# Kernel tuning notes

Measured on AMD Instinct MI355X. Metric: run time of the kernel, lower is better.

The kernel has to match this reference:

```python
import jax, jax.numpy as jnp
import numpy as np

BIGNET_DIM = 1024
N_LAYERS = 18   # 6 blocks * 3 QLoRALinear
N_LN = 5
GROUPS = 64     # 1024 / group_size(16)
GS = 16
RANK = 32
BATCH = 16384
EPS = 1e-5


def dequant(qw, scale):
    # qw: [O, G, gs] int 0..15, scale: [O, G] per-group max-abs norm
    w = (qw.astype(jnp.float32) / 15.0 * 2.0 - 1.0) * scale[..., None]
    return w.reshape(qw.shape[0], -1)  # [O, I]


def qlora_linear(x, qw, scale, b, a_w, b_w):
    w = dequant(qw, scale)                      # [O, I]
    base = x @ w.T + b                          # [N, O]
    lora = (x @ a_w.T) @ b_w.T                  # [N, r] @ [r, O]
    return base + lora


def layernorm(h, g, b):
    mu = h.mean(-1, keepdims=True)
    var = jnp.mean((h - mu) ** 2, -1, keepdims=True)
    return (h - mu) * jax.lax.rsqrt(var + EPS) * g + b


def setup_inputs() -> dict:
    key = jax.random.key(0)
    ks = jax.random.split(key, 8)
    x = jax.random.normal(ks[0], (BATCH, BIGNET_DIM), jnp.float32)
    qw = jax.random.randint(ks[1], (N_LAYERS, BIGNET_DIM, GROUPS, GS), 0, 16, jnp.int32)
    scale = jax.random.uniform(ks[2], (N_LAYERS, BIGNET_DIM, GROUPS), jnp.float32) * 0.05
    bias = jax.random.normal(ks[3], (N_LAYERS, BIGNET_DIM), jnp.float32) * 0.02
    la = jax.random.normal(ks[4], (N_LAYERS, RANK, BIGNET_DIM), jnp.float32) * (2.0 / BIGNET_DIM) ** 0.5
    # note: torch zero-inits lora_b; use small random values so the LoRA path is testable
    lb = jax.random.normal(ks[5], (N_LAYERS, BIGNET_DIM, RANK), jnp.float32) * 0.01
    ln_w = jnp.ones((N_LN, BIGNET_DIM), jnp.float32)
    ln_b = jnp.zeros((N_LN, BIGNET_DIM), jnp.float32)
    return {"x": x, "scale": scale, "bias": bias, "la": la, "lb": lb,
            "ln_w": ln_w, "ln_b": ln_b, "qw": qw}


def reference(x, scale, bias, la, lb, ln_w, ln_b, qw):
    h = x
    li = 0
    for blk in range(6):
        r = h
        for j in range(3):
            h = qlora_linear(h, qw[li], scale[li], bias[li], la[li], lb[li])
            li += 1
            if j < 2:
                h = jax.nn.relu(h)
        h = h + r
        if blk < 5:
            h = layernorm(h, ln_w[blk], ln_b[blk])
    return h
```

## Files before the change

kernel.cpp:

```cpp
#include <hip/hip_runtime.h>

typedef unsigned short UST;
typedef __attribute__((ext_vector_type(8))) __bf16 bf16x8;
typedef __attribute__((ext_vector_type(4))) float f32x4;

__device__ __forceinline__ float bf2f(UST u) {
    union { unsigned int i; float f; } v; v.i = ((unsigned int)u) << 16; return v.f;
}
__device__ __forceinline__ UST f2bf(float f) {
    union { float f; unsigned int i; } v; v.f = f;
    return (UST)((v.i + 0x7fffu + ((v.i >> 16) & 1u)) >> 16);
}

__device__ __forceinline__ void gl2lds16(const UST* g, UST* l) {
    __builtin_amdgcn_global_load_lds(
        (const __attribute__((address_space(1))) unsigned int*)g,
        (__attribute__((address_space(3))) unsigned int*)l, 16, 0, 0);
}

#define WB4 asm volatile("s_waitcnt vmcnt(4)\n\ts_barrier" ::: "memory")
#define WB0 asm volatile("s_waitcnt vmcnt(0)\n\ts_barrier" ::: "memory")
#define LGB asm volatile("s_waitcnt lgkmcnt(0)\n\ts_barrier" ::: "memory")

__global__ __launch_bounds__(256) void prep_w(
    const int* __restrict__ qw, const float* __restrict__ scale,
    const float* __restrict__ la, const float* __restrict__ lb,
    UST* __restrict__ wp)
{
    int l = blockIdx.x, ot = blockIdx.y, it = blockIdx.z;
    __shared__ float buf[8192];
    __shared__ float sc_s[128 * 8];
    int t = threadIdx.x;
    int wave = t >> 6, lane = t & 63;
    int wm = wave >> 1, wn = wave & 1;
    int la15 = lane & 15, qa = lane >> 4;

    {
        int e = t * 4;
        int o = e >> 3, g = e & 7;
        const float* sb = scale + ((size_t)l * 1024 + ot * 128 + o) * 64 + it * 8 + g;
        *(float4*)&sc_s[e] = *(const float4*)sb;
    }

    float* last = buf;
    {
        const float* laB = la + (size_t)l * 32 * 1024 + it * 128;
        #pragma unroll
        for (int p = 0; p < 4; p++) {
            int e = t * 4 + p * 1024;
            int r = e >> 7, i0 = e & 127;
            float4 v = *(const float4*)(laB + (size_t)r * 1024 + i0);
            last[(i0 + 0) * 33 + r] = v.x;
            last[(i0 + 1) * 33 + r] = v.y;
            last[(i0 + 2) * 33 + r] = v.z;
            last[(i0 + 3) * 33 + r] = v.w;
        }
    }

    bf16x8 af[4];
    const float* lbL = lb + ((size_t)l * 1024 + ot * 128 + wm * 64 + la15) * 32 + qa * 8;
    #pragma unroll
    for (int mi = 0; mi < 4; mi++) {
        float4 u0 = *(const float4*)(lbL + mi * 16 * 32);
        float4 u1 = *(const float4*)(lbL + mi * 16 * 32 + 4);
        union { bf16x8 v; UST u[8]; } A;
        A.u[0] = f2bf(u0.x); A.u[1] = f2bf(u0.y); A.u[2] = f2bf(u0.z); A.u[3] = f2bf(u0.w);
        A.u[4] = f2bf(u1.x); A.u[5] = f2bf(u1.y); A.u[6] = f2bf(u1.z); A.u[7] = f2bf(u1.w);
        af[mi] = A.v;
    }

    __syncthreads();

    bf16x8 bfr[4];
    #pragma unroll
    for (int ni = 0; ni < 4; ni++) {
        int iloc = wn * 64 + ni * 16 + la15;
        const float* pp = &last[iloc * 33 + qa * 8];
        union { bf16x8 v; UST u[8]; } B;
        #pragma unroll
        for (int j = 0; j < 8; j++) B.u[j] = f2bf(pp[j]);
        bfr[ni] = B.v;
    }

    f32x4 acc[4][4];
    #pragma unroll
    for (int mi = 0; mi < 4; mi++)
        #pragma unroll
        for (int ni = 0; ni < 4; ni++) {
            acc[mi][ni] = (f32x4){0.f, 0.f, 0.f, 0.f};
            acc[mi][ni] = __builtin_amdgcn_mfma_f32_16x16x32_bf16(
                af[mi], bfr[ni], acc[mi][ni], 0, 0, 0);
        }

    __syncthreads();

    float* cs = buf;
    int cc = t & 15, rw = t >> 4;
    UST* wL = wp + (size_t)l * 1048576;
    const int* qL = qw + (size_t)l * 1048576;
    #pragma unroll
    for (int h = 0; h < 2; ++h) {
        int4 qd[4][2];
        #pragma unroll
        for (int g = 0; g < 4; g++) {
            int rl = g * 16 + rw;
            const int* qrow = qL + (size_t)(ot * 128 + h * 64 + rl) * 1024
                              + it * 128 + cc * 8;
            qd[g][0] = *(const int4*)qrow;
            qd[g][1] = *(const int4*)(qrow + 4);
        }
        if (wm == h) {
            #pragma unroll
            for (int mi = 0; mi < 4; mi++)
                #pragma unroll
                for (int ni = 0; ni < 4; ni++) {
                    int colx = (wn * 64 + ni * 16 + la15) ^ (qa << 4);
                    #pragma unroll
                    for (int r2 = 0; r2 < 4; r2++) {
                        int rl = mi * 16 + qa * 4 + r2;
                        cs[rl * 128 + colx] = acc[mi][ni][r2];
                    }
                }
        }
        LGB;
        #pragma unroll
        for (int g = 0; g < 4; ++g) {
            int rl = g * 16 + rw;
            int swz = ((rl >> 2) & 3) << 2;
            int gr0 = ((cc * 2) ^ swz) * 4;
            float4 v0 = *(const float4*)&cs[rl * 128 + gr0];
            float4 v1 = *(const float4*)&cs[rl * 128 + gr0 + 4];
            float s = sc_s[(h * 64 + rl) * 8 + (cc >> 1)];
            float t2 = s * (2.0f / 15.0f);
            float o0 = fmaf((float)qd[g][0].x, t2, v0.x - s);
            float o1 = fmaf((float)qd[g][0].y, t2, v0.y - s);
            float o2 = fmaf((float)qd[g][0].z, t2, v0.z - s);
            float o3 = fmaf((float)qd[g][0].w, t2, v0.w - s);
            float o4 = fmaf((float)qd[g][1].x, t2, v1.x - s);
            float o5 = fmaf((float)qd[g][1].y, t2, v1.y - s);
            float o6 = fmaf((float)qd[g][1].z, t2, v1.z - s);
            float o7 = fmaf((float)qd[g][1].w, t2, v1.w - s);
            uint4 pk;
            pk.x = (unsigned)f2bf(o0) | ((unsigned)f2bf(o1) << 16);
            pk.y = (unsigned)f2bf(o2) | ((unsigned)f2bf(o3) << 16);
            pk.z = (unsigned)f2bf(o4) | ((unsigned)f2bf(o5) << 16);
            pk.w = (unsigned)f2bf(o6) | ((unsigned)f2bf(o7) << 16);
            *(uint4*)&wL[(size_t)(ot * 128 + h * 64 + rl) * 1024 + it * 128 + cc * 8] = pk;
        }
        LGB;
    }
}

__global__ __launch_bounds__(256) void f32_to_bf16(const float* __restrict__ x,
                                                   UST* __restrict__ o)
{
    size_t i = ((size_t)blockIdx.x * 256 + threadIdx.x) * 4;
    float4 v = *(const float4*)(x + i);
    *(ushort4*)(o + i) = make_ushort4(f2bf(v.x), f2bf(v.y), f2bf(v.z), f2bf(v.w));
}

#define BK 32

__global__ __launch_bounds__(512, 2) void gemm_ep(
    const UST* __restrict__ X, const UST* __restrict__ W,
    const float* __restrict__ bias,
    UST* __restrict__ outb, const UST* __restrict__ resid,
    float* __restrict__ outf, int mode)
{
    const int K = 1024;
    __shared__ UST smem[32768];
    int tid = threadIdx.x;
    int wave = tid >> 6, lane = tid & 63;
    int wm = wave >> 1, wn = wave & 1;
    int la15 = lane & 15, qa = lane >> 4;

    int bid = blockIdx.x;
    int xcd = bid & 7, idx = bid >> 3;
    int bm = xcd * 8 + (idx & 7);
    int bn = idx >> 3;

    int c0 = tid, c1 = tid + 512;
    int r0 = c0 >> 2, k0c = ((c0 & 3) ^ ((r0 >> 1) & 3)) * 8;
    int r1 = c1 >> 2, k1c = ((c1 & 3) ^ ((r1 >> 1) & 3)) * 8;
    const UST* gA0 = X + (size_t)(bm * 256 + r0) * K + k0c;
    const UST* gA1 = X + (size_t)(bm * 256 + r1) * K + k1c;
    const UST* gB0 = W + (size_t)(bn * 256 + r0) * K + k0c;
    const UST* gB1 = W + (size_t)(bn * 256 + r1) * K + k1c;

    int offA[4], offB[8];
    #pragma unroll
    for (int i = 0; i < 4; i++) {
        int ra = wm * 64 + i * 16 + la15;
        offA[i] = ra * 32 + ((qa ^ ((ra >> 1) & 3)) * 8);
    }
    #pragma unroll
    for (int i = 0; i < 8; i++) {
        int rb = wn * 128 + i * 16 + la15;
        offB[i] = rb * 32 + ((qa ^ ((rb >> 1) & 3)) * 8);
    }

    f32x4 acc[4][8];
    #pragma unroll
    for (int i = 0; i < 4; i++)
        #pragma unroll
        for (int j = 0; j < 8; j++) acc[i][j] = (f32x4){0.f, 0.f, 0.f, 0.f};

    auto issue = [&](int kk, int buf) {
        UST* dA = smem + buf * 16384;
        UST* dB = dA + 8192;
        gl2lds16(gA0 + kk, dA + c0 * 8);
        gl2lds16(gA1 + kk, dA + c1 * 8);
        gl2lds16(gB0 + kk, dB + c0 * 8);
        gl2lds16(gB1 + kk, dB + c1 * 8);
    };
    auto compute = [&](int buf) {
        const UST* pA = smem + buf * 16384;
        const UST* pB = pA + 8192;
        bf16x8 af[4], bfr[8];
        #pragma unroll
        for (int mi = 0; mi < 4; mi++) af[mi] = *(const bf16x8*)&pA[offA[mi]];
        #pragma unroll
        for (int ni = 0; ni < 8; ni++) bfr[ni] = *(const bf16x8*)&pB[offB[ni]];
        #pragma unroll
        for (int mi = 0; mi < 4; mi++)
            #pragma unroll
            for (int ni = 0; ni < 8; ni++)
                acc[mi][ni] = __builtin_amdgcn_mfma_f32_16x16x32_bf16(
                    af[mi], bfr[ni], acc[mi][ni], 0, 0, 0);
    };

    issue(0, 0);
    #pragma unroll 2
    for (int it = 0; it < 31; ++it) {
        int cur = it & 1;
        issue((it + 1) * BK, cur ^ 1);
        WB4;
        compute(cur);
        LGB;
    }
    WB0;
    compute(1);
    LGB;

    float* cs = (float*)smem;
    int cc = tid & 31, rw = tid >> 5;
    int gcolb = bn * 256 + cc * 8;
    float4 bv0 = *(const float4*)&bias[gcolb];
    float4 bv1 = *(const float4*)&bias[gcolb + 4];

    #pragma unroll
    for (int h = 0; h < 4; ++h) {
        if (wm == h) {
            #pragma unroll
            for (int mi = 0; mi < 4; mi++)
                #pragma unroll
                for (int ni = 0; ni < 8; ni++) {
                    int colx = (wn * 128 + ni * 16 + la15) ^ (qa << 4);
                    #pragma unroll
                    for (int r2 = 0; r2 < 4; r2++) {
                        int rl = mi * 16 + qa * 4 + r2;
                        cs[rl * 256 + colx] = acc[mi][ni][r2];
                    }
                }
        }
        LGB;
        #pragma unroll
        for (int g = 0; g < 4; ++g) {
            int rl = g * 16 + rw;
            int swz = ((rl >> 2) & 3) << 2;
            int gr0 = ((cc * 2) ^ swz) * 4;
            float4 v0 = *(const float4*)&cs[rl * 256 + gr0];
            float4 v1 = *(const float4*)&cs[rl * 256 + gr0 + 4];
            float o0 = v0.x + bv0.x, o1 = v0.y + bv0.y;
            float o2 = v0.z + bv0.z, o3 = v0.w + bv0.w;
            float o4 = v1.x + bv1.x, o5 = v1.y + bv1.y;
            float o6 = v1.z + bv1.z, o7 = v1.w + bv1.w;
            if (mode == 0) {
                o0 = fmaxf(o0, 0.f); o1 = fmaxf(o1, 0.f);
                o2 = fmaxf(o2, 0.f); o3 = fmaxf(o3, 0.f);
                o4 = fmaxf(o4, 0.f); o5 = fmaxf(o5, 0.f);
                o6 = fmaxf(o6, 0.f); o7 = fmaxf(o7, 0.f);
            }
            int grow = bm * 256 + h * 64 + rl;
            size_t base = (size_t)grow * 1024 + gcolb;
            if (mode != 0) {
                ushort4 rv0 = *(const ushort4*)&resid[base];
                ushort4 rv1 = *(const ushort4*)&resid[base + 4];
                o0 += bf2f(rv0.x); o1 += bf2f(rv0.y);
                o2 += bf2f(rv0.z); o3 += bf2f(rv0.w);
                o4 += bf2f(rv1.x); o5 += bf2f(rv1.y);
                o6 += bf2f(rv1.z); o7 += bf2f(rv1.w);
            }
            if (mode == 2) {
                *(float4*)&outf[base] = make_float4(o0, o1, o2, o3);
                *(float4*)&outf[base + 4] = make_float4(o4, o5, o6, o7);
            } else {
                uint4 pk;
                pk.x = (unsigned)f2bf(o0) | ((unsigned)f2bf(o1) << 16);
                pk.y = (unsigned)f2bf(o2) | ((unsigned)f2bf(o3) << 16);
                pk.z = (unsigned)f2bf(o4) | ((unsigned)f2bf(o5) << 16);
                pk.w = (unsigned)f2bf(o6) | ((unsigned)f2bf(o7) << 16);
                *(uint4*)&outb[base] = pk;
            }
        }
        LGB;
    }
}

__global__ __launch_bounds__(256) void ln_only(
    const UST* __restrict__ s, UST* __restrict__ r,
    const float* __restrict__ g, const float* __restrict__ b)
{
    int wave = threadIdx.x >> 6, lane = threadIdx.x & 63;
    int row = blockIdx.x * 4 + wave;
    const UST* sp = s + (size_t)row * 1024;
    UST* rp = r + (size_t)row * 1024;

    float v[16];
    float sum = 0.f, ss = 0.f;
    #pragma unroll
    for (int k = 0; k < 4; k++) {
        ushort4 hv = *(const ushort4*)(sp + k * 256 + lane * 4);
        float a0 = bf2f(hv.x), a1 = bf2f(hv.y), a2 = bf2f(hv.z), a3 = bf2f(hv.w);
        v[k * 4 + 0] = a0; v[k * 4 + 1] = a1; v[k * 4 + 2] = a2; v[k * 4 + 3] = a3;
        sum += a0 + a1 + a2 + a3;
        ss += a0 * a0 + a1 * a1 + a2 * a2 + a3 * a3;
    }
    #pragma unroll
    for (int off = 32; off > 0; off >>= 1) {
        sum += __shfl_down(sum, off, 64);
        ss  += __shfl_down(ss, off, 64);
    }
    sum = __shfl(sum, 0, 64);
    ss  = __shfl(ss, 0, 64);
    float mean = sum * (1.0f / 1024.0f);
    float var = ss * (1.0f / 1024.0f) - mean * mean;
    float rstd = rsqrtf(var + 1e-5f);

    #pragma unroll
    for (int k = 0; k < 4; k++) {
        int c = k * 256 + lane * 4;
        float4 gv = *(const float4*)(g + c);
        float4 bv = *(const float4*)(b + c);
        ushort4 o;
        o.x = f2bf((v[k * 4 + 0] - mean) * rstd * gv.x + bv.x);
        o.y = f2bf((v[k * 4 + 1] - mean) * rstd * gv.y + bv.y);
        o.z = f2bf((v[k * 4 + 2] - mean) * rstd * gv.z + bv.z);
        o.w = f2bf((v[k * 4 + 3] - mean) * rstd * gv.w + bv.w);
        *(ushort4*)(rp + c) = o;
    }
}

extern "C" void kernel_launch(void* const* d_in, const int* in_sizes, int n_in,
                              void* d_out, int out_size, void* d_ws, size_t ws_size,
                              hipStream_t stream) {
    const float* x     = (const float*)d_in[0];
    const float* scale = (const float*)d_in[1];
    const float* bias  = (const float*)d_in[2];
    const float* la    = (const float*)d_in[3];
    const float* lb    = (const float*)d_in[4];
    const float* ln_w  = (const float*)d_in[5];
    const float* ln_b  = (const float*)d_in[6];
    const int*   qw    = (const int*)d_in[7];

    const int M = in_sizes[0] / 1024;
    const size_t WPB = (size_t)18 * 1024 * 1024 * 2;
    const size_t ACT = (size_t)M * 1024 * 2;

    UST* wp = (UST*)d_ws;
    UST* A  = (UST*)((char*)d_ws + WPB);
    UST* Cb = (UST*)((char*)d_ws + WPB + ACT);
    UST* Bb = (UST*)d_out;

    prep_w<<<dim3(18, 8, 8), 256, 0, stream>>>(qw, scale, la, lb, wp);
    f32_to_bf16<<<(M * 1024) / (256 * 4), 256, 0, stream>>>(x, A);

    int nblk = (M / 256) * 4;
    int li = 0;
    for (int blk = 0; blk < 6; ++blk) {
        gemm_ep<<<nblk, 512, 0, stream>>>(
            A, wp + (size_t)li * 1024 * 1024, bias + li * 1024, Bb, nullptr, nullptr, 0);
        li++;
        gemm_ep<<<nblk, 512, 0, stream>>>(
            Bb, wp + (size_t)li * 1024 * 1024, bias + li * 1024, Cb, nullptr, nullptr, 0);
        li++;
        if (blk < 5) {
            gemm_ep<<<nblk, 512, 0, stream>>>(
                Cb, wp + (size_t)li * 1024 * 1024, bias + li * 1024, Bb, A, nullptr, 1);
            li++;
            ln_only<<<M / 4, 256, 0, stream>>>(Bb, A, ln_w + blk * 1024, ln_b + blk * 1024);
        } else {
            gemm_ep<<<nblk, 512, 0, stream>>>(
                Cb, wp + (size_t)li * 1024 * 1024, bias + li * 1024, nullptr, A,
                (float*)d_out, 2);
            li++;
        }
    }
}
```

Baseline: 940.9 us.

## Shrink GEMM tile to 128x256 with 256-thread blocks and raise MFMA priority

```diff
diff --git a/kernel.cpp b/kernel.cpp
--- a/kernel.cpp
+++ b/kernel.cpp
@@ -18,7 +18,7 @@
         (__attribute__((address_space(3))) unsigned int*)l, 16, 0, 0);
 }
 
-#define WB4 asm volatile("s_waitcnt vmcnt(4)\n\ts_barrier" ::: "memory")
+#define WB6 asm volatile("s_waitcnt vmcnt(6)\n\ts_barrier" ::: "memory")
 #define WB0 asm volatile("s_waitcnt vmcnt(0)\n\ts_barrier" ::: "memory")
 #define LGB asm volatile("s_waitcnt lgkmcnt(0)\n\ts_barrier" ::: "memory")
 
@@ -161,14 +161,14 @@
 
 #define BK 32
 
-__global__ __launch_bounds__(512, 2) void gemm_ep(
+__global__ __launch_bounds__(256, 2) void gemm_ep(
     const UST* __restrict__ X, const UST* __restrict__ W,
     const float* __restrict__ bias,
     UST* __restrict__ outb, const UST* __restrict__ resid,
     float* __restrict__ outf, int mode)
 {
     const int K = 1024;
-    __shared__ UST smem[32768];
+    __shared__ UST smem[24576];
     int tid = threadIdx.x;
     int wave = tid >> 6, lane = tid & 63;
     int wm = wave >> 1, wn = wave & 1;
@@ -176,16 +176,23 @@
 
     int bid = blockIdx.x;
     int xcd = bid & 7, idx = bid >> 3;
-    int bm = xcd * 8 + (idx & 7);
-    int bn = idx >> 3;
-
-    int c0 = tid, c1 = tid + 512;
-    int r0 = c0 >> 2, k0c = ((c0 & 3) ^ ((r0 >> 1) & 3)) * 8;
-    int r1 = c1 >> 2, k1c = ((c1 & 3) ^ ((r1 >> 1) & 3)) * 8;
-    const UST* gA0 = X + (size_t)(bm * 256 + r0) * K + k0c;
-    const UST* gA1 = X + (size_t)(bm * 256 + r1) * K + k1c;
-    const UST* gB0 = W + (size_t)(bn * 256 + r0) * K + k0c;
-    const UST* gB1 = W + (size_t)(bn * 256 + r1) * K + k1c;
+    int bm = xcd * 16 + (idx & 15);
+    int bn = idx >> 4;
+
+    int a0 = tid, a1 = tid + 256;
+    int rA0 = a0 >> 2, kA0 = ((a0 & 3) ^ ((rA0 >> 1) & 3)) * 8;
+    int rA1 = a1 >> 2, kA1 = ((a1 & 3) ^ ((rA1 >> 1) & 3)) * 8;
+    const UST* gA0 = X + (size_t)(bm * 128 + rA0) * K + kA0;
+    const UST* gA1 = X + (size_t)(bm * 128 + rA1) * K + kA1;
+    int b0 = tid, b1 = tid + 256, b2 = tid + 512, b3 = tid + 768;
+    int rB0 = b0 >> 2, kB0 = ((b0 & 3) ^ ((rB0 >> 1) & 3)) * 8;
+    int rB1 = b1 >> 2, kB1 = ((b1 & 3) ^ ((rB1 >> 1) & 3)) * 8;
+    int rB2 = b2 >> 2, kB2 = ((b2 & 3) ^ ((rB2 >> 1) & 3)) * 8;
+    int rB3 = b3 >> 2, kB3 = ((b3 & 3) ^ ((rB3 >> 1) & 3)) * 8;
+    const UST* gB0 = W + (size_t)(bn * 256 + rB0) * K + kB0;
+    const UST* gB1 = W + (size_t)(bn * 256 + rB1) * K + kB1;
+    const UST* gB2 = W + (size_t)(bn * 256 + rB2) * K + kB2;
+    const UST* gB3 = W + (size_t)(bn * 256 + rB3) * K + kB3;
 
     int offA[4], offB[8];
     #pragma unroll
@@ -206,27 +213,31 @@
         for (int j = 0; j < 8; j++) acc[i][j] = (f32x4){0.f, 0.f, 0.f, 0.f};
 
     auto issue = [&](int kk, int buf) {
-        UST* dA = smem + buf * 16384;
-        UST* dB = dA + 8192;
-        gl2lds16(gA0 + kk, dA + c0 * 8);
-        gl2lds16(gA1 + kk, dA + c1 * 8);
-        gl2lds16(gB0 + kk, dB + c0 * 8);
-        gl2lds16(gB1 + kk, dB + c1 * 8);
+        UST* dA = smem + buf * 12288;
+        UST* dB = dA + 4096;
+        gl2lds16(gA0 + kk, dA + a0 * 8);
+        gl2lds16(gA1 + kk, dA + a1 * 8);
+        gl2lds16(gB0 + kk, dB + b0 * 8);
+        gl2lds16(gB1 + kk, dB + b1 * 8);
+        gl2lds16(gB2 + kk, dB + b2 * 8);
+        gl2lds16(gB3 + kk, dB + b3 * 8);
     };
     auto compute = [&](int buf) {
-        const UST* pA = smem + buf * 16384;
-        const UST* pB = pA + 8192;
+        const UST* pA = smem + buf * 12288;
+        const UST* pB = pA + 4096;
         bf16x8 af[4], bfr[8];
         #pragma unroll
         for (int mi = 0; mi < 4; mi++) af[mi] = *(const bf16x8*)&pA[offA[mi]];
         #pragma unroll
         for (int ni = 0; ni < 8; ni++) bfr[ni] = *(const bf16x8*)&pB[offB[ni]];
+        __builtin_amdgcn_s_setprio(1);
         #pragma unroll
         for (int mi = 0; mi < 4; mi++)
             #pragma unroll
             for (int ni = 0; ni < 8; ni++)
                 acc[mi][ni] = __builtin_amdgcn_mfma_f32_16x16x32_bf16(
                     af[mi], bfr[ni], acc[mi][ni], 0, 0, 0);
+        __builtin_amdgcn_s_setprio(0);
     };
 
     issue(0, 0);
@@ -234,7 +245,7 @@
     for (int it = 0; it < 31; ++it) {
         int cur = it & 1;
         issue((it + 1) * BK, cur ^ 1);
-        WB4;
+        WB6;
         compute(cur);
         LGB;
     }
@@ -249,24 +260,26 @@
     float4 bv1 = *(const float4*)&bias[gcolb + 4];
 
     #pragma unroll
-    for (int h = 0; h < 4; ++h) {
-        if (wm == h) {
+    for (int s = 0; s < 4; ++s) {
+        if (wm == (s >> 1)) {
             #pragma unroll
-            for (int mi = 0; mi < 4; mi++)
+            for (int mh = 0; mh < 2; mh++) {
+                int mi = (s & 1) * 2 + mh;
                 #pragma unroll
                 for (int ni = 0; ni < 8; ni++) {
                     int colx = (wn * 128 + ni * 16 + la15) ^ (qa << 4);
                     #pragma unroll
                     for (int r2 = 0; r2 < 4; r2++) {
-                        int rl = mi * 16 + qa * 4 + r2;
+                        int rl = mh * 16 + qa * 4 + r2;
                         cs[rl * 256 + colx] = acc[mi][ni][r2];
                     }
                 }
+            }
         }
         LGB;
         #pragma unroll
         for (int g = 0; g < 4; ++g) {
-            int rl = g * 16 + rw;
+            int rl = g * 8 + rw;
             int swz = ((rl >> 2) & 3) << 2;
             int gr0 = ((cc * 2) ^ swz) * 4;
             float4 v0 = *(const float4*)&cs[rl * 256 + gr0];
@@ -281,7 +294,7 @@
                 o4 = fmaxf(o4, 0.f); o5 = fmaxf(o5, 0.f);
                 o6 = fmaxf(o6, 0.f); o7 = fmaxf(o7, 0.f);
             }
-            int grow = bm * 256 + h * 64 + rl;
+            int grow = bm * 128 + s * 32 + rl;
             size_t base = (size_t)grow * 1024 + gcolb;
             if (mode != 0) {
                 ushort4 rv0 = *(const ushort4*)&resid[base];
@@ -375,22 +388,22 @@
     prep_w<<<dim3(18, 8, 8), 256, 0, stream>>>(qw, scale, la, lb, wp);
     f32_to_bf16<<<(M * 1024) / (256 * 4), 256, 0, stream>>>(x, A);
 
-    int nblk = (M / 256) * 4;
+    int nblk = (M / 128) * 4;
     int li = 0;
     for (int blk = 0; blk < 6; ++blk) {
-        gemm_ep<<<nblk, 512, 0, stream>>>(
+        gemm_ep<<<nblk, 256, 0, stream>>>(
             A, wp + (size_t)li * 1024 * 1024, bias + li * 1024, Bb, nullptr, nullptr, 0);
         li++;
-        gemm_ep<<<nblk, 512, 0, stream>>>(
+        gemm_ep<<<nblk, 256, 0, stream>>>(
             Bb, wp + (size_t)li * 1024 * 1024, bias + li * 1024, Cb, nullptr, nullptr, 0);
         li++;
         if (blk < 5) {
-            gemm_ep<<<nblk, 512, 0, stream>>>(
+            gemm_ep<<<nblk, 256, 0, stream>>>(
                 Cb, wp + (size_t)li * 1024 * 1024, bias + li * 1024, Bb, A, nullptr, 1);
             li++;
             ln_only<<<M / 4, 256, 0, stream>>>(Bb, A, ln_w + blk * 1024, ln_b + blk * 1024);
         } else {
-            gemm_ep<<<nblk, 512, 0, stream>>>(
+            gemm_ep<<<nblk, 256, 0, stream>>>(
                 Cb, wp + (size_t)li * 1024 * 1024, bias + li * 1024, nullptr, A,
                 (float*)d_out, 2);
             li++;
```

After: 1.007 ms. 1.07x slower.

## Deepen GEMM to 4-stage LDS pipeline with split A/B prefetch and 2x4 wave layout

Applied to the files above, without the earlier changes.

```diff
diff --git a/kernel.cpp b/kernel.cpp
--- a/kernel.cpp
+++ b/kernel.cpp
@@ -18,9 +18,13 @@
         (__attribute__((address_space(3))) unsigned int*)l, 16, 0, 0);
 }
 
-#define WB4 asm volatile("s_waitcnt vmcnt(4)\n\ts_barrier" ::: "memory")
-#define WB0 asm volatile("s_waitcnt vmcnt(0)\n\ts_barrier" ::: "memory")
-#define LGB asm volatile("s_waitcnt lgkmcnt(0)\n\ts_barrier" ::: "memory")
+#define WBAR8 asm volatile("s_waitcnt vmcnt(8)\n\ts_barrier" ::: "memory")
+#define WBAR4 asm volatile("s_waitcnt vmcnt(4)\n\ts_barrier" ::: "memory")
+#define WBAR0 asm volatile("s_waitcnt vmcnt(0)\n\ts_barrier" ::: "memory")
+#define BAR   asm volatile("s_barrier" ::: "memory")
+#define LGB   asm volatile("s_waitcnt lgkmcnt(0)\n\ts_barrier" ::: "memory")
+#define LGW   do { asm volatile("s_waitcnt lgkmcnt(0)" ::: "memory"); \
+                   __builtin_amdgcn_sched_barrier(0); } while (0)
 
 __global__ __launch_bounds__(256) void prep_w(
     const int* __restrict__ qw, const float* __restrict__ scale,
@@ -168,10 +172,10 @@
     float* __restrict__ outf, int mode)
 {
     const int K = 1024;
-    __shared__ UST smem[32768];
+    __shared__ UST smem[65536];
     int tid = threadIdx.x;
     int wave = tid >> 6, lane = tid & 63;
-    int wm = wave >> 1, wn = wave & 1;
+    int wm = wave >> 2, wn = wave & 3;
     int la15 = lane & 15, qa = lane >> 4;
 
     int bid = blockIdx.x;
@@ -187,59 +191,80 @@
     const UST* gB0 = W + (size_t)(bn * 256 + r0) * K + k0c;
     const UST* gB1 = W + (size_t)(bn * 256 + r1) * K + k1c;
 
-    int offA[4], offB[8];
+    int offA[8], offB[4];
+    #pragma unroll
+    for (int i = 0; i < 8; i++) {
+        int ra = wm * 128 + i * 16 + la15;
+        offA[i] = ra * 32 + ((qa ^ ((ra >> 1) & 3)) * 8);
+    }
     #pragma unroll
     for (int i = 0; i < 4; i++) {
-        int ra = wm * 64 + i * 16 + la15;
-        offA[i] = ra * 32 + ((qa ^ ((ra >> 1) & 3)) * 8);
-    }
-    #pragma unroll
-    for (int i = 0; i < 8; i++) {
-        int rb = wn * 128 + i * 16 + la15;
+        int rb = wn * 64 + i * 16 + la15;
         offB[i] = rb * 32 + ((qa ^ ((rb >> 1) & 3)) * 8);
     }
 
-    f32x4 acc[4][8];
-    #pragma unroll
-    for (int i = 0; i < 4; i++)
-        #pragma unroll
-        for (int j = 0; j < 8; j++) acc[i][j] = (f32x4){0.f, 0.f, 0.f, 0.f};
-
-    auto issue = [&](int kk, int buf) {
-        UST* dA = smem + buf * 16384;
-        UST* dB = dA + 8192;
-        gl2lds16(gA0 + kk, dA + c0 * 8);
-        gl2lds16(gA1 + kk, dA + c1 * 8);
-        gl2lds16(gB0 + kk, dB + c0 * 8);
-        gl2lds16(gB1 + kk, dB + c1 * 8);
+    f32x4 acc[8][4];
+    #pragma unroll
+    for (int i = 0; i < 8; i++)
+        #pragma unroll
+        for (int j = 0; j < 4; j++) acc[i][j] = (f32x4){0.f, 0.f, 0.f, 0.f};
+
+    auto stageA = [&](int s) {
+        UST* sA = smem + (s & 3) * 16384;
+        gl2lds16(gA0 + s * BK, sA + c0 * 8);
+        gl2lds16(gA1 + s * BK, sA + c1 * 8);
     };
-    auto compute = [&](int buf) {
-        const UST* pA = smem + buf * 16384;
-        const UST* pB = pA + 8192;
-        bf16x8 af[4], bfr[8];
-        #pragma unroll
-        for (int mi = 0; mi < 4; mi++) af[mi] = *(const bf16x8*)&pA[offA[mi]];
-        #pragma unroll
-        for (int ni = 0; ni < 8; ni++) bfr[ni] = *(const bf16x8*)&pB[offB[ni]];
-        #pragma unroll
-        for (int mi = 0; mi < 4; mi++)
-            #pragma unroll
-            for (int ni = 0; ni < 8; ni++)
-                acc[mi][ni] = __builtin_amdgcn_mfma_f32_16x16x32_bf16(
-                    af[mi], bfr[ni], acc[mi][ni], 0, 0, 0);
+    auto stageB = [&](int s) {
+        UST* sB = smem + (s & 3) * 16384 + 8192;
+        gl2lds16(gB0 + s * BK, sB + c0 * 8);
+        gl2lds16(gB1 + s * BK, sB + c1 * 8);
     };
 
-    issue(0, 0);
-    #pragma unroll 2
-    for (int it = 0; it < 31; ++it) {
-        int cur = it & 1;
-        issue((it + 1) * BK, cur ^ 1);
-        WB4;
-        compute(cur);
-        LGB;
-    }
-    WB0;
-    compute(1);
+    stageA(0); stageB(0);
+    stageA(1); stageB(1);
+    stageA(2); stageB(2);
+
+#define STEPBODY(s, WAITM, DOST)                                            \
+    {                                                                       \
+        const UST* pA = smem + ((s) & 3) * 16384;                           \
+        const UST* pB = pA + 8192;                                          \
+        WAITM;                                             \
+        bf16x8 af0[4], bfn[4];                                              \
+        _Pragma("unroll")                                                   \
+        for (int mi = 0; mi < 4; mi++) af0[mi] = *(const bf16x8*)&pA[offA[mi]]; \
+        _Pragma("unroll")                                                   \
+        for (int ni = 0; ni < 4; ni++) bfn[ni] = *(const bf16x8*)&pB[offB[ni]]; \
+        if (DOST) stageA((s) + 3);                                          \
+        LGW;                                                                \
+        __builtin_amdgcn_s_setprio(1);                                      \
+        _Pragma("unroll")                                                   \
+        for (int mi = 0; mi < 4; mi++)                                      \
+            _Pragma("unroll")                                               \
+            for (int ni = 0; ni < 4; ni++)                                  \
+                acc[mi][ni] = __builtin_amdgcn_mfma_f32_16x16x32_bf16(      \
+                    af0[mi], bfn[ni], acc[mi][ni], 0, 0, 0);                \
+        __builtin_amdgcn_s_setprio(0);                                      \
+        BAR;                                                                \
+        bf16x8 af1[4];                                                      \
+        _Pragma("unroll")                                                   \
+        for (int mi = 0; mi < 4; mi++) af1[mi] = *(const bf16x8*)&pA[offA[4 + mi]]; \
+        if (DOST) stageB((s) + 3);                                          \
+        LGW;                                                                \
+        __builtin_amdgcn_s_setprio(1);                                      \
+        _Pragma("unroll")                                                   \
+        for (int mi = 0; mi < 4; mi++)                                      \
+            _Pragma("unroll")                                               \
+            for (int ni = 0; ni < 4; ni++)                                  \
+                acc[4 + mi][ni] = __builtin_amdgcn_mfma_f32_16x16x32_bf16(  \
+                    af1[mi], bfn[ni], acc[4 + mi][ni], 0, 0, 0);            \
+        __builtin_amdgcn_s_setprio(0);                                      \
+    }
+
+    for (int s = 0; s < 29; ++s) STEPBODY(s, WBAR8, 1);
+    STEPBODY(29, WBAR8, 0);
+    STEPBODY(30, WBAR4, 0);
+    STEPBODY(31, WBAR0, 0);
+#undef STEPBODY
     LGB;
 
     float* cs = (float*)smem;
@@ -250,18 +275,20 @@
 
     #pragma unroll
     for (int h = 0; h < 4; ++h) {
-        if (wm == h) {
+        if (wm == (h >> 1)) {
             #pragma unroll
-            for (int mi = 0; mi < 4; mi++)
+            for (int m = 0; m < 4; m++) {
+                int mi = (h & 1) * 4 + m;
                 #pragma unroll
-                for (int ni = 0; ni < 8; ni++) {
-                    int colx = (wn * 128 + ni * 16 + la15) ^ (qa << 4);
+                for (int ni = 0; ni < 4; ni++) {
+                    int colx = (wn * 64 + ni * 16 + la15) ^ (qa << 4);
                     #pragma unroll
                     for (int r2 = 0; r2 < 4; r2++) {
-                        int rl = mi * 16 + qa * 4 + r2;
+                        int rl = m * 16 + qa * 4 + r2;
                         cs[rl * 256 + colx] = acc[mi][ni][r2];
                     }
                 }
+            }
         }
         LGB;
         #pragma unroll
```

New measurement: 929.9 us. About the same (-1.2%).

## Make each block own a 64-row stripe across all output columns, streaming weights

Applied to the files above, without the earlier changes.

```diff
diff --git a/kernel.cpp b/kernel.cpp
--- a/kernel.cpp
+++ b/kernel.cpp
@@ -18,8 +18,6 @@
         (__attribute__((address_space(3))) unsigned int*)l, 16, 0, 0);
 }
 
-#define WB4 asm volatile("s_waitcnt vmcnt(4)\n\ts_barrier" ::: "memory")
-#define WB0 asm volatile("s_waitcnt vmcnt(0)\n\ts_barrier" ::: "memory")
 #define LGB asm volatile("s_waitcnt lgkmcnt(0)\n\ts_barrier" ::: "memory")
 
 __global__ __launch_bounds__(256) void prep_w(
@@ -159,8 +157,6 @@
     *(ushort4*)(o + i) = make_ushort4(f2bf(v.x), f2bf(v.y), f2bf(v.z), f2bf(v.w));
 }
 
-#define BK 32
-
 __global__ __launch_bounds__(512, 2) void gemm_ep(
     const UST* __restrict__ X, const UST* __restrict__ W,
     const float* __restrict__ bias,
@@ -168,36 +164,34 @@
     float* __restrict__ outf, int mode)
 {
     const int K = 1024;
-    __shared__ UST smem[32768];
+    __shared__ UST smem[65536];
     int tid = threadIdx.x;
-    int wave = tid >> 6, lane = tid & 63;
-    int wm = wave >> 1, wn = wave & 1;
+    int wv = tid >> 6, lane = tid & 63;
     int la15 = lane & 15, qa = lane >> 4;
 
     int bid = blockIdx.x;
-    int xcd = bid & 7, idx = bid >> 3;
-    int bm = xcd * 8 + (idx & 7);
-    int bn = idx >> 3;
-
-    int c0 = tid, c1 = tid + 512;
-    int r0 = c0 >> 2, k0c = ((c0 & 3) ^ ((r0 >> 1) & 3)) * 8;
-    int r1 = c1 >> 2, k1c = ((c1 & 3) ^ ((r1 >> 1) & 3)) * 8;
-    const UST* gA0 = X + (size_t)(bm * 256 + r0) * K + k0c;
-    const UST* gA1 = X + (size_t)(bm * 256 + r1) * K + k1c;
-    const UST* gB0 = W + (size_t)(bn * 256 + r0) * K + k0c;
-    const UST* gB1 = W + (size_t)(bn * 256 + r1) * K + k1c;
-
-    int offA[4], offB[8];
-    #pragma unroll
-    for (int i = 0; i < 4; i++) {
-        int ra = wm * 64 + i * 16 + la15;
-        offA[i] = ra * 32 + ((qa ^ ((ra >> 1) & 3)) * 8);
-    }
-    #pragma unroll
-    for (int i = 0; i < 8; i++) {
-        int rb = wn * 128 + i * 16 + la15;
-        offB[i] = rb * 32 + ((qa ^ ((rb >> 1) & 3)) * 8);
-    }
+    int bm = (bid & 7) * 32 + (bid >> 3);
+
+    {
+        const UST* xb = X + (size_t)bm * 64 * K;
+        #pragma unroll
+        for (int j = 0; j < 16; j++) {
+            int c = tid + j * 512;
+            int row = c >> 7, slot = c & 127;
+            int ks = slot ^ (row & 7);
+            gl2lds16(xb + (size_t)row * K + ks * 8, smem + c * 8);
+        }
+    }
+
+    const UST* gB[8];
+    #pragma unroll
+    for (int ni = 0; ni < 8; ni++)
+        gB[ni] = W + (size_t)(wv * 128 + ni * 16 + la15) * K + qa * 8;
+
+    int rowb[4];
+    int e = la15 & 7;
+    #pragma unroll
+    for (int mi = 0; mi < 4; mi++) rowb[mi] = (mi * 16 + la15) * 1024;
 
     f32x4 acc[4][8];
     #pragma unroll
@@ -205,57 +199,41 @@
         #pragma unroll
         for (int j = 0; j < 8; j++) acc[i][j] = (f32x4){0.f, 0.f, 0.f, 0.f};
 
-    auto issue = [&](int kk, int buf) {
-        UST* dA = smem + buf * 16384;
-        UST* dB = dA + 8192;
-        gl2lds16(gA0 + kk, dA + c0 * 8);
-        gl2lds16(gA1 + kk, dA + c1 * 8);
-        gl2lds16(gB0 + kk, dB + c0 * 8);
-        gl2lds16(gB1 + kk, dB + c1 * 8);
-    };
-    auto compute = [&](int buf) {
-        const UST* pA = smem + buf * 16384;
-        const UST* pB = pA + 8192;
-        bf16x8 af[4], bfr[8];
-        #pragma unroll
-        for (int mi = 0; mi < 4; mi++) af[mi] = *(const bf16x8*)&pA[offA[mi]];
-        #pragma unroll
-        for (int ni = 0; ni < 8; ni++) bfr[ni] = *(const bf16x8*)&pB[offB[ni]];
+    __syncthreads();
+
+    #pragma unroll 8
+    for (int t = 0; t < 32; ++t) {
+        bf16x8 bf[8], af[4];
+        #pragma unroll
+        for (int ni = 0; ni < 8; ni++)
+            bf[ni] = *(const bf16x8*)(gB[ni] + t * 32);
+        #pragma unroll
+        for (int mi = 0; mi < 4; mi++) {
+            int ks = (t * 4 + qa) ^ e;
+            af[mi] = *(const bf16x8*)&smem[rowb[mi] + ks * 8];
+        }
         #pragma unroll
         for (int mi = 0; mi < 4; mi++)
             #pragma unroll
             for (int ni = 0; ni < 8; ni++)
                 acc[mi][ni] = __builtin_amdgcn_mfma_f32_16x16x32_bf16(
-                    af[mi], bfr[ni], acc[mi][ni], 0, 0, 0);
-    };
-
-    issue(0, 0);
-    #pragma unroll 2
-    for (int it = 0; it < 31; ++it) {
-        int cur = it & 1;
-        issue((it + 1) * BK, cur ^ 1);
-        WB4;
-        compute(cur);
-        LGB;
-    }
-    WB0;
-    compute(1);
+                    af[mi], bf[ni], acc[mi][ni], 0, 0, 0);
+    }
+
     LGB;
 
     float* cs = (float*)smem;
     int cc = tid & 31, rw = tid >> 5;
-    int gcolb = bn * 256 + cc * 8;
-    float4 bv0 = *(const float4*)&bias[gcolb];
-    float4 bv1 = *(const float4*)&bias[gcolb + 4];
-
-    #pragma unroll
-    for (int h = 0; h < 4; ++h) {
-        if (wm == h) {
+
+    #pragma unroll
+    for (int s = 0; s < 4; ++s) {
+        if ((wv >> 1) == s) {
+            int ch = (wv & 1) * 128;
             #pragma unroll
             for (int mi = 0; mi < 4; mi++)
                 #pragma unroll
                 for (int ni = 0; ni < 8; ni++) {
-                    int colx = (wn * 128 + ni * 16 + la15) ^ (qa << 4);
+                    int colx = ch + ((ni * 16 + la15) ^ (qa << 4));
                     #pragma unroll
                     for (int r2 = 0; r2 < 4; r2++) {
                         int rl = mi * 16 + qa * 4 + r2;
@@ -264,6 +242,9 @@
                 }
         }
         LGB;
+        int gcolb = s * 256 + cc * 8;
+        float4 bv0 = *(const float4*)&bias[gcolb];
+        float4 bv1 = *(const float4*)&bias[gcolb + 4];
         #pragma unroll
         for (int g = 0; g < 4; ++g) {
             int rl = g * 16 + rw;
@@ -281,7 +262,7 @@
                 o4 = fmaxf(o4, 0.f); o5 = fmaxf(o5, 0.f);
                 o6 = fmaxf(o6, 0.f); o7 = fmaxf(o7, 0.f);
             }
-            int grow = bm * 256 + h * 64 + rl;
+            int grow = bm * 64 + rl;
             size_t base = (size_t)grow * 1024 + gcolb;
             if (mode != 0) {
                 ushort4 rv0 = *(const ushort4*)&resid[base];
@@ -375,7 +356,7 @@
     prep_w<<<dim3(18, 8, 8), 256, 0, stream>>>(qw, scale, la, lb, wp);
     f32_to_bf16<<<(M * 1024) / (256 * 4), 256, 0, stream>>>(x, A);
 
-    int nblk = (M / 256) * 4;
+    int nblk = M / 64;
     int li = 0;
     for (int blk = 0; blk < 6; ++blk) {
         gemm_ep<<<nblk, 512, 0, stream>>>(
```

Result: slower. 1.598 ms (+69.8%).
